# Kernel optimization log

Hardware: AMD Instinct MI355X
Metric: run time of the kernel (lower is better)

Reference implementation:

```python
import jax, jax.numpy as jnp
import numpy as np

NUM_HEADS = 4
CATEGORY_SIZE = 128
NUM_TOKENS = 64


def setup_inputs() -> dict:
    key = jax.random.key(0)
    k1, k2, k3 = jax.random.split(key, 3)
    b, n, c = 2, 65536, 192
    qkv = jax.random.normal(k1, (b, n, 3 * c), dtype=jnp.float32)
    sim = jax.random.normal(k2, (b, n, NUM_TOKENS), dtype=jnp.float32)
    proj_w = jax.random.normal(k3, (c, c), dtype=jnp.float32) * 0.02  # nn.Linear weight (out, in)
    proj_b = jnp.zeros((c,), dtype=jnp.float32)
    logit_scale = jnp.log(10.0) * jnp.ones((1, 1), dtype=jnp.float32)
    return {"qkv": qkv, "sim": sim, "proj_w": proj_w, "proj_b": proj_b,
            "logit_scale": logit_scale, "H": 256, "W": 256}


def reference(qkv, sim, proj_w, proj_b, logit_scale, H, W):
    b, n, c3 = qkv.shape
    c = c3 // 3
    hd = c // NUM_HEADS
    gs = min(n, CATEGORY_SIZE)
    ng = (n + gs - 1) // gs
    pad_n = ng * gs - n

    # cluster id per token, sort tokens by cluster (dynamic reorder)
    tk_id = jnp.argmax(sim, axis=-1)                    # (b, n) int
    sort_idx = jnp.argsort(tk_id, axis=-1)              # permutation
    rev_idx = jnp.argsort(sort_idx, axis=-1)            # inverse permutation (index_reverse)

    shuffled = jnp.take_along_axis(qkv, sort_idx[..., None], axis=1)  # (b, n, 3c)
    if pad_n > 0:
        pad = shuffled[:, n - pad_n:n][:, ::-1]         # torch.flip of tail
        shuffled = jnp.concatenate([shuffled, pad], axis=1)

    # (b, ng, gs, 3, nh, hd) -> (3, b, ng, nh, gs, hd)
    y = shuffled.reshape(b, ng, gs, 3, NUM_HEADS, hd)
    qkv_g = jnp.transpose(y, (3, 0, 1, 4, 2, 5))
    q, k, v = qkv_g[0], qkv_g[1], qkv_g[2]

    # clamped learned logit scale (no normalization in original code)
    scale = jnp.exp(jnp.minimum(logit_scale, jnp.log(1.0 / 0.01)))[0, 0]
    attn = jnp.einsum('bgnsd,bgntd->bgnst', q, k) * scale   # (b, ng, nh, gs, gs)
    attn = jax.nn.softmax(attn, axis=-1)
    out = jnp.einsum('bgnst,bgntd->bgnsd', attn, v)         # (b, ng, nh, gs, hd)

    out = jnp.transpose(out, (0, 1, 3, 2, 4)).reshape(b, ng * gs, c)[:, :n]
    x = jnp.take_along_axis(out, rev_idx[..., None], axis=1)  # unshuffle
    x = x @ proj_w.T + proj_b
    return x
```

## Files before the change

kernel.cpp:

```cpp
#include <hip/hip_runtime.h>

#define B_  2
#define N_  65536
#define C_  192
#define NH_ 4
#define HD_ 48
#define GS_ 128
#define NG_ 512
#define NTILES_ 256

typedef __attribute__((ext_vector_type(8))) short short8;
typedef __attribute__((ext_vector_type(4))) float f32x4;

__device__ __forceinline__ unsigned short f2bf(float f) {
    unsigned u = __float_as_uint(f);
    unsigned r = (u + 0x7FFFu + ((u >> 16) & 1u)) >> 16;
    return (unsigned short)r;
}
__device__ __forceinline__ float bf2f(unsigned short s) {
    return __uint_as_float(((unsigned)s) << 16);
}
__device__ __forceinline__ unsigned cvt_pk(float a, float b) {
    unsigned r;
    asm("v_cvt_pk_bf16_f32 %0, %1, %2" : "=v"(r) : "v"(a), "v"(b));
    return r;
}

__global__ __launch_bounds__(256) void argmax_kernel(const float* __restrict__ sim,
                                                     int* __restrict__ keys) {
    int lane  = threadIdx.x & 63;
    int token = blockIdx.x * 4 + (threadIdx.x >> 6);
    float v = sim[(size_t)token * 64 + lane];
    int idx = lane;
    #pragma unroll
    for (int m = 1; m < 64; m <<= 1) {
        float ov = __shfl_xor(v, m);
        int   oi = __shfl_xor(idx, m);
        if (ov > v || (ov == v && oi < idx)) { v = ov; idx = oi; }
    }
    if (lane == 0) keys[token] = idx;
}

__global__ __launch_bounds__(256) void hist_kernel(const int* __restrict__ keys,
                                                   int* __restrict__ counts) {
    __shared__ int hcnt[64];
    int tid  = threadIdx.x;
    int tile = blockIdx.x & (NTILES_ - 1);
    int bz   = blockIdx.x >> 8;
    if (tid < 64) hcnt[tid] = 0;
    __syncthreads();
    int k = keys[bz * N_ + tile * 256 + tid];
    atomicAdd(&hcnt[k], 1);
    __syncthreads();
    if (tid < 64) counts[(bz * NTILES_ + tile) * 64 + tid] = hcnt[tid];
}

__global__ __launch_bounds__(256) void scan_kernel(int* __restrict__ counts) {
    __shared__ int qsum[4][64];
    __shared__ int kbase[64];
    int bz = blockIdx.x;
    int k  = threadIdx.x & 63;
    int qt = threadIdx.x >> 6;
    int base_idx = (bz * NTILES_) * 64 + k;

    int sum = 0;
    #pragma unroll 8
    for (int t = qt * 64; t < qt * 64 + 64; ++t) sum += counts[base_idx + t * 64];
    qsum[qt][k] = sum;
    __syncthreads();

    if (qt == 0) {
        int tot = qsum[0][k] + qsum[1][k] + qsum[2][k] + qsum[3][k];
        int incl = tot;
        #pragma unroll
        for (int off = 1; off < 64; off <<= 1) {
            int v = __shfl_up(incl, off);
            if (k >= off) incl += v;
        }
        kbase[k] = incl - tot;
    }
    __syncthreads();

    int run = kbase[k];
    for (int q2 = 0; q2 < qt; ++q2) run += qsum[q2][k];
    #pragma unroll 8
    for (int t = qt * 64; t < qt * 64 + 64; ++t) {
        int idx = base_idx + t * 64;
        int c = counts[idx];
        counts[idx] = run;
        run += c;
    }
}

__global__ __launch_bounds__(256) void rank_kernel(const int* __restrict__ keys,
                                                   const int* __restrict__ counts,
                                                   int* __restrict__ sidx,
                                                   int* __restrict__ dest) {
    __shared__ int whist[4 * 64];
    int tid  = threadIdx.x;
    int tile = blockIdx.x & (NTILES_ - 1);
    int bz   = blockIdx.x >> 8;
    whist[tid] = 0;
    __syncthreads();

    int tok = tile * 256 + tid;
    int key = keys[bz * N_ + tok];
    int w = tid >> 6, lane = tid & 63;

    unsigned long long mask = ~0ull;
    #pragma unroll
    for (int b = 0; b < 6; ++b) {
        unsigned long long bb = __ballot((key >> b) & 1);
        mask &= ((key >> b) & 1) ? bb : ~bb;
    }
    unsigned long long lt = (lane == 0) ? 0ull : (~0ull >> (64 - lane));
    int rank = __popcll(mask & lt);
    if (rank == 0) whist[w * 64 + key] = __popcll(mask);
    __syncthreads();

    int base = counts[(bz * NTILES_ + tile) * 64 + key];
    for (int w2 = 0; w2 < w; ++w2) base += whist[w2 * 64 + key];
    int pos = base + rank;
    sidx[bz * N_ + pos] = tok;
    dest[bz * N_ + tok] = pos;
}

#define KP_STRIDE 104
#define P_STRIDE  136
#define VT_STRIDE 136
#define SM_VT   34816
#define SM_SIDX (SM_VT + 48*VT_STRIDE*2)
#define SM_SIZE (SM_SIDX + 512)

__global__ __launch_bounds__(256, 3) void attn_kernel(const float* __restrict__ qkv,
                                                      const float* __restrict__ lscale,
                                                      const int* __restrict__ sort_idx,
                                                      unsigned short* __restrict__ oattn) {
    __shared__ __align__(16) char smem[SM_SIZE];
    unsigned short* kp = (unsigned short*)smem;
    unsigned short* vt = (unsigned short*)(smem + SM_VT);
    int* sidx_s = (int*)(smem + SM_SIDX);

    int x  = blockIdx.x;
    int h  = x & 3;
    int g  = (x >> 2) & (NG_ - 1);
    int bz = x >> 11;
    int tid = threadIdx.x;

    if (tid < 128) sidx_s[tid] = sort_idx[bz * N_ + g * GS_ + tid];
    __syncthreads();

    int lane = tid & 63, wid = tid >> 6;
    int lr = lane & 15, lg = lane >> 4;
    int qt0 = wid * 2, qt1 = qt0 + 1;
    float scale = __expf(fminf(lscale[0], 4.60517019f));

    int r0s = lg * 8;
    int r1s = 16 + lg * 8;
    int r2s = (lg < 2) ? 32 + lg * 8 : (lg - 2) * 8;
    const float* q0p = qkv + (size_t)(bz * N_ + sidx_s[qt0 * 16 + lr]) * 576 + h * 48;
    const float* q1p = qkv + (size_t)(bz * N_ + sidx_s[qt1 * 16 + lr]) * 576 + h * 48;
    float4 qA0 = *(const float4*)(q0p + r0s), qA1 = *(const float4*)(q0p + r0s + 4);
    float4 qB0 = *(const float4*)(q0p + r1s), qB1 = *(const float4*)(q0p + r1s + 4);
    float4 qC0 = *(const float4*)(q0p + r2s), qC1 = *(const float4*)(q0p + r2s + 4);
    float4 pA0 = *(const float4*)(q1p + r0s), pA1 = *(const float4*)(q1p + r0s + 4);
    float4 pB0 = *(const float4*)(q1p + r1s), pB1 = *(const float4*)(q1p + r1s + 4);
    float4 pC0 = *(const float4*)(q1p + r2s), pC1 = *(const float4*)(q1p + r2s + 4);

    #pragma unroll
    for (int it = 0; it < 6; ++it) {
        int f = it * 256 + tid;
        int row = f / 12, piece = f - row * 12;
        float4 kf = *(const float4*)(qkv + (size_t)(bz * N_ + sidx_s[row]) * 576 + 192 + h * 48 + piece * 4);
        unsigned h01 = cvt_pk(kf.x, kf.y), h23 = cvt_pk(kf.z, kf.w);
        float hx = __uint_as_float(h01 << 16), hy = __uint_as_float(h01 & 0xFFFF0000u);
        float hz = __uint_as_float(h23 << 16), hw = __uint_as_float(h23 & 0xFFFF0000u);
        unsigned l01 = cvt_pk(kf.x - hx, kf.y - hy), l23 = cvt_pk(kf.z - hz, kf.w - hw);
        *(uint2*)(kp + row * KP_STRIDE + piece * 4)      = make_uint2(h01, h23);
        *(uint2*)(kp + row * KP_STRIDE + 48 + piece * 4) = make_uint2(l01, l23);
    }
    #pragma unroll
    for (int it = 0; it < 6; ++it) {
        int f = it * 256 + tid;
        int row = f / 12, piece = f - row * 12;
        float4 vf = *(const float4*)(qkv + (size_t)(bz * N_ + sidx_s[row]) * 576 + 384 + h * 48 + piece * 4);
        int d = piece * 4;
        vt[(d + 0) * VT_STRIDE + row] = f2bf(vf.x);
        vt[(d + 1) * VT_STRIDE + row] = f2bf(vf.y);
        vt[(d + 2) * VT_STRIDE + row] = f2bf(vf.z);
        vt[(d + 3) * VT_STRIDE + row] = f2bf(vf.w);
    }

    unsigned af0[5][4], af1[5][4];
    {
        float a0[8] = {qA0.x,qA0.y,qA0.z,qA0.w,qA1.x,qA1.y,qA1.z,qA1.w};
        float b0[8] = {qB0.x,qB0.y,qB0.z,qB0.w,qB1.x,qB1.y,qB1.z,qB1.w};
        float c0[8] = {qC0.x,qC0.y,qC0.z,qC0.w,qC1.x,qC1.y,qC1.z,qC1.w};
        float a1[8] = {pA0.x,pA0.y,pA0.z,pA0.w,pA1.x,pA1.y,pA1.z,pA1.w};
        float b1[8] = {pB0.x,pB0.y,pB0.z,pB0.w,pB1.x,pB1.y,pB1.z,pB1.w};
        float c1[8] = {pC0.x,pC0.y,pC0.z,pC0.w,pC1.x,pC1.y,pC1.z,pC1.w};
        #pragma unroll
        for (int j = 0; j < 8; ++j) {
            a0[j] *= scale; b0[j] *= scale; c0[j] *= scale;
            a1[j] *= scale; b1[j] *= scale; c1[j] *= scale;
        }
        #pragma unroll
        for (int w = 0; w < 4; ++w) {
            af0[0][w] = cvt_pk(a0[2*w], a0[2*w+1]);
            af1[0][w] = cvt_pk(a1[2*w], a1[2*w+1]);
            af0[3][w] = af0[0][w];
            af1[3][w] = af1[0][w];
            {
                unsigned t0 = cvt_pk(b0[2*w], b0[2*w+1]);
                float hx = __uint_as_float(t0 << 16), hy = __uint_as_float(t0 & 0xFFFF0000u);
                af0[2][w] = cvt_pk(b0[2*w] - hx, b0[2*w+1] - hy);
                unsigned t1 = cvt_pk(b1[2*w], b1[2*w+1]);
                float ix = __uint_as_float(t1 << 16), iy = __uint_as_float(t1 & 0xFFFF0000u);
                af1[2][w] = cvt_pk(b1[2*w] - ix, b1[2*w+1] - iy);
            }
            if (lg < 2) {
                af0[1][w] = cvt_pk(c0[2*w], c0[2*w+1]);
                af1[1][w] = cvt_pk(c1[2*w], c1[2*w+1]);
                af0[4][w] = af0[1][w];
                af1[4][w] = af1[1][w];
            } else {
                unsigned t0 = cvt_pk(c0[2*w], c0[2*w+1]);
                float hx = __uint_as_float(t0 << 16), hy = __uint_as_float(t0 & 0xFFFF0000u);
                af0[1][w] = cvt_pk(c0[2*w] - hx, c0[2*w+1] - hy);
                unsigned t1 = cvt_pk(c1[2*w], c1[2*w+1]);
                float ix = __uint_as_float(t1 << 16), iy = __uint_as_float(t1 & 0xFFFF0000u);
                af1[1][w] = cvt_pk(c1[2*w] - ix, c1[2*w+1] - iy);
                af0[4][w] = 0; af1[4][w] = 0;
            }
        }
    }
    __syncthreads();

    const int boffs[5] = { lg * 8, (32 + lg * 8) % 48, 16 + lg * 8,
                           48 + lg * 8, (lg < 2) ? 80 + lg * 8 : 48 };
    f32x4 acc0[8], acc1[8];
    #pragma unroll
    for (int kt = 0; kt < 8; ++kt) { acc0[kt] = (f32x4)0.f; acc1[kt] = (f32x4)0.f; }

    #pragma unroll
    for (int s = 0; s < 5; ++s) {
        union { short8 v; unsigned u[4]; } ua, ub;
        #pragma unroll
        for (int w = 0; w < 4; ++w) { ua.u[w] = af0[s][w]; ub.u[w] = af1[s][w]; }
        short8 a0 = ua.v, a1 = ub.v;
        #pragma unroll
        for (int kt = 0; kt < 8; ++kt) {
            short8 b = *(const short8*)(kp + (size_t)(kt * 16 + lr) * KP_STRIDE + boffs[s]);
            acc0[kt] = __builtin_amdgcn_mfma_f32_16x16x32_bf16(a0, b, acc0[kt], 0, 0, 0);
            acc1[kt] = __builtin_amdgcn_mfma_f32_16x16x32_bf16(a1, b, acc1[kt], 0, 0, 0);
        }
    }

    float inv0[4], inv1[4];
    {
        float mx0[4], mx1[4];
        #pragma unroll
        for (int r = 0; r < 4; ++r) { mx0[r] = -1e30f; mx1[r] = -1e30f; }
        #pragma unroll
        for (int kt = 0; kt < 8; ++kt)
            #pragma unroll
            for (int r = 0; r < 4; ++r) {
                mx0[r] = fmaxf(mx0[r], acc0[kt][r]);
                mx1[r] = fmaxf(mx1[r], acc1[kt][r]);
            }
        #pragma unroll
        for (int m = 1; m < 16; m <<= 1)
            #pragma unroll
            for (int r = 0; r < 4; ++r) {
                mx0[r] = fmaxf(mx0[r], __shfl_xor(mx0[r], m));
                mx1[r] = fmaxf(mx1[r], __shfl_xor(mx1[r], m));
            }
        float sm0[4] = {0.f,0.f,0.f,0.f}, sm1[4] = {0.f,0.f,0.f,0.f};
        #pragma unroll
        for (int kt = 0; kt < 8; ++kt)
            #pragma unroll
            for (int r = 0; r < 4; ++r) {
                float e0 = __expf(acc0[kt][r] - mx0[r]);
                float e1 = __expf(acc1[kt][r] - mx1[r]);
                acc0[kt][r] = e0; acc1[kt][r] = e1;
                sm0[r] += e0; sm1[r] += e1;
            }
        #pragma unroll
        for (int m = 1; m < 16; m <<= 1)
            #pragma unroll
            for (int r = 0; r < 4; ++r) {
                sm0[r] += __shfl_xor(sm0[r], m);
                sm1[r] += __shfl_xor(sm1[r], m);
            }
        #pragma unroll
        for (int r = 0; r < 4; ++r) { inv0[r] = 1.f / sm0[r]; inv1[r] = 1.f / sm1[r]; }
    }

    __syncthreads();

    #pragma unroll
    for (int kt = 0; kt < 8; ++kt)
        #pragma unroll
        for (int r = 0; r < 4; ++r) {
            kp[(size_t)(qt0 * 16 + lg * 4 + r) * P_STRIDE + kt * 16 + lr] = (unsigned short)cvt_pk(acc0[kt][r], acc0[kt][r]);
            kp[(size_t)(qt1 * 16 + lg * 4 + r) * P_STRIDE + kt * 16 + lr] = (unsigned short)cvt_pk(acc1[kt][r], acc1[kt][r]);
        }

    f32x4 o0[3], o1[3];
    #pragma unroll
    for (int dt = 0; dt < 3; ++dt) { o0[dt] = (f32x4)0.f; o1[dt] = (f32x4)0.f; }
    #pragma unroll
    for (int ks = 0; ks < 4; ++ks) {
        short8 a0 = *(const short8*)(kp + (size_t)(qt0 * 16 + lr) * P_STRIDE + ks * 32 + lg * 8);
        short8 a1 = *(const short8*)(kp + (size_t)(qt1 * 16 + lr) * P_STRIDE + ks * 32 + lg * 8);
        #pragma unroll
        for (int dt = 0; dt < 3; ++dt) {
            short8 bv = *(const short8*)(vt + (size_t)(dt * 16 + lr) * VT_STRIDE + ks * 32 + lg * 8);
            o0[dt] = __builtin_amdgcn_mfma_f32_16x16x32_bf16(a0, bv, o0[dt], 0, 0, 0);
            o1[dt] = __builtin_amdgcn_mfma_f32_16x16x32_bf16(a1, bv, o1[dt], 0, 0, 0);
        }
    }

    #pragma unroll
    for (int dt = 0; dt < 3; ++dt)
        #pragma unroll
        for (int r = 0; r < 4; ++r) {
            int row0 = qt0 * 16 + lg * 4 + r;
            int row1 = qt1 * 16 + lg * 4 + r;
            oattn[(size_t)(bz * N_ + g * GS_ + row0) * C_ + h * HD_ + dt * 16 + lr] =
                f2bf(o0[dt][r] * inv0[r]);
            oattn[(size_t)(bz * N_ + g * GS_ + row1) * C_ + h * HD_ + dt * 16 + lr] =
                f2bf(o1[dt][r] * inv1[r]);
        }
}

__global__ __launch_bounds__(256) void wconv_kernel(const float* __restrict__ W,
                                                    unsigned short* __restrict__ wbf) {
    int i = blockIdx.x * 256 + threadIdx.x;
    float4 f = ((const float4*)W)[i];
    uint2 p;
    p.x = (unsigned)f2bf(f.x) | ((unsigned)f2bf(f.y) << 16);
    p.y = (unsigned)f2bf(f.z) | ((unsigned)f2bf(f.w) << 16);
    ((uint2*)wbf)[i] = p;
}

__global__ __launch_bounds__(256) void proj2_kernel(const unsigned short* __restrict__ oattn,
                                                    const int* __restrict__ dest,
                                                    const unsigned short* __restrict__ wbf,
                                                    const float* __restrict__ bias,
                                                    float* __restrict__ out) {
    __shared__ int mpos[128];
    int tid = threadIdx.x;
    int m0  = blockIdx.x * 128;

    if (tid < 128) {
        int m = m0 + tid;
        int bz = m >> 16;
        mpos[tid] = bz * N_ + dest[m];
    }
    __syncthreads();

    int lane = tid & 63, wid = tid >> 6;
    int lr = lane & 15, lg = lane >> 4;
    int mt0 = wid * 2, mt1 = wid * 2 + 1;

    const unsigned short* xr0 = oattn + (size_t)mpos[mt0 * 16 + lr] * C_ + lg * 8;
    const unsigned short* xr1 = oattn + (size_t)mpos[mt1 * 16 + lr] * C_ + lg * 8;
    const unsigned short* wr  = wbf + (size_t)lr * C_ + lg * 8;

    f32x4 acc[2][12];
    #pragma unroll
    for (int mt = 0; mt < 2; ++mt)
        #pragma unroll
        for (int jt = 0; jt < 12; ++jt) acc[mt][jt] = (f32x4)0.f;

    #pragma unroll
    for (int ks = 0; ks < 6; ++ks) {
        short8 a0 = *(const short8*)(xr0 + ks * 32);
        short8 a1 = *(const short8*)(xr1 + ks * 32);
        #pragma unroll
        for (int jt = 0; jt < 12; ++jt) {
            short8 b = *(const short8*)(wr + (size_t)jt * 16 * C_ + ks * 32);
            acc[0][jt] = __builtin_amdgcn_mfma_f32_16x16x32_bf16(a0, b, acc[0][jt], 0, 0, 0);
            acc[1][jt] = __builtin_amdgcn_mfma_f32_16x16x32_bf16(a1, b, acc[1][jt], 0, 0, 0);
        }
    }

    #pragma unroll
    for (int jt = 0; jt < 12; ++jt) {
        int j = jt * 16 + lr;
        float bj = bias[j];
        #pragma unroll
        for (int r = 0; r < 4; ++r) {
            int row0 = m0 + mt0 * 16 + lg * 4 + r;
            int row1 = m0 + mt1 * 16 + lg * 4 + r;
            out[(size_t)row0 * C_ + j] = acc[0][jt][r] + bj;
            out[(size_t)row1 * C_ + j] = acc[1][jt][r] + bj;
        }
    }
}

extern "C" void kernel_launch(void* const* d_in, const int* in_sizes, int n_in,
                              void* d_out, int out_size, void* d_ws, size_t ws_size,
                              hipStream_t stream) {
    const float* qkv    = (const float*)d_in[0];
    const float* sim    = (const float*)d_in[1];
    const float* proj_w = (const float*)d_in[2];
    const float* proj_b = (const float*)d_in[3];
    const float* lscale = (const float*)d_in[4];
    float* out = (float*)d_out;

    char* ws = (char*)d_ws;
    int* keys   = (int*)(ws);
    int* dest   = (int*)(ws + 524288);
    int* sidx   = (int*)(ws + 1048576);
    int* counts = (int*)(ws + 1572864);
    unsigned short* oattn = (unsigned short*)(ws + 1703936);
    unsigned short* wbf   = (unsigned short*)(ws + 1703936 + 50331648);

    argmax_kernel<<<32768, 256, 0, stream>>>(sim, keys);
    hist_kernel<<<B_ * NTILES_, 256, 0, stream>>>(keys, counts);
    scan_kernel<<<B_, 256, 0, stream>>>(counts);
    rank_kernel<<<B_ * NTILES_, 256, 0, stream>>>(keys, counts, sidx, dest);
    wconv_kernel<<<36, 256, 0, stream>>>(proj_w, wbf);
    attn_kernel<<<B_ * NG_ * NH_, 256, 0, stream>>>(qkv, lscale, sidx, oattn);
    proj2_kernel<<<(B_ * N_) / 128, 256, 0, stream>>>(oattn, dest, wbf, proj_b, out);
}
```

Before: 216.4 us.

## Keep softmax probabilities in registers, swap QK operands, reorder block mapping, scatter proj output

The QK^T MFMA now takes K as the A operand and Q as B, so each lane holds a full probability column. That column is normalized, packed to bf16 in registers, and fed straight into 16x16x16 MFMAs for PV. This removes the LDS round-trip for P, a __syncthreads, and the 16-lane shuffle reductions. The smaller LDS footprint allows launch bounds of 4 blocks per SM, and block indices are remapped so that 8 consecutive blocks share the same head. proj2 now reads oattn contiguously in sorted order and scatters its output rows through sidx, which removes the dest array and its writes in rank_kernel. The risks are more register pressure and scattered fp32 output writes.

Result: no change. 218.7 us (+1.0%).

```diff
diff --git a/kernel.cpp b/kernel.cpp
--- a/kernel.cpp
+++ b/kernel.cpp
@@ -10,6 +10,7 @@
 #define NTILES_ 256
 
 typedef __attribute__((ext_vector_type(8))) short short8;
+typedef __attribute__((ext_vector_type(4))) short short4v;
 typedef __attribute__((ext_vector_type(4))) float f32x4;
 
 __device__ __forceinline__ unsigned short f2bf(float f) {
@@ -24,6 +25,22 @@
     unsigned r;
     asm("v_cvt_pk_bf16_f32 %0, %1, %2" : "=v"(r) : "v"(a), "v"(b));
     return r;
+}
+
+#if defined(__has_builtin)
+#if __has_builtin(__builtin_amdgcn_mfma_f32_16x16x16bf16_1k)
+#define HAVE_MFMA16_1K 1
+#endif
+#endif
+__device__ __forceinline__ f32x4 mfma16(short4v a, short4v b, f32x4 c) {
+#ifdef HAVE_MFMA16_1K
+    return __builtin_amdgcn_mfma_f32_16x16x16bf16_1k(a, b, c, 0, 0, 0);
+#else
+    f32x4 d;
+    asm volatile("v_mfma_f32_16x16x16_bf16 %0, %1, %2, %3"
+                 : "=&v"(d) : "v"(a), "v"(b), "v"(c));
+    return d;
+#endif
 }
 
 __global__ __launch_bounds__(256) void argmax_kernel(const float* __restrict__ sim,
@@ -94,8 +111,7 @@
 
 __global__ __launch_bounds__(256) void rank_kernel(const int* __restrict__ keys,
                                                    const int* __restrict__ counts,
-                                                   int* __restrict__ sidx,
-                                                   int* __restrict__ dest) {
+                                                   int* __restrict__ sidx) {
     __shared__ int whist[4 * 64];
     int tid  = threadIdx.x;
     int tile = blockIdx.x & (NTILES_ - 1);
@@ -122,29 +138,28 @@
     for (int w2 = 0; w2 < w; ++w2) base += whist[w2 * 64 + key];
     int pos = base + rank;
     sidx[bz * N_ + pos] = tok;
-    dest[bz * N_ + tok] = pos;
 }
 
 #define KP_STRIDE 104
-#define P_STRIDE  136
-#define VT_STRIDE 136
-#define SM_VT   34816
-#define SM_SIDX (SM_VT + 48*VT_STRIDE*2)
-#define SM_SIZE (SM_SIDX + 512)
-
-__global__ __launch_bounds__(256, 3) void attn_kernel(const float* __restrict__ qkv,
+#define VT_STRIDE 132
+#define KP_BYTES  (128 * KP_STRIDE * 2)
+#define VT_BYTES  (48 * VT_STRIDE * 2)
+#define SM_SIZE   (KP_BYTES + VT_BYTES + 512)
+
+__global__ __launch_bounds__(256, 4) void attn_kernel(const float* __restrict__ qkv,
                                                       const float* __restrict__ lscale,
                                                       const int* __restrict__ sort_idx,
                                                       unsigned short* __restrict__ oattn) {
     __shared__ __align__(16) char smem[SM_SIZE];
     unsigned short* kp = (unsigned short*)smem;
-    unsigned short* vt = (unsigned short*)(smem + SM_VT);
-    int* sidx_s = (int*)(smem + SM_SIDX);
+    unsigned short* vt = (unsigned short*)(smem + KP_BYTES);
+    int* sidx_s = (int*)(smem + KP_BYTES + VT_BYTES);
 
     int x  = blockIdx.x;
-    int h  = x & 3;
-    int g  = (x >> 2) & (NG_ - 1);
-    int bz = x >> 11;
+    int gg = (x & 7) | ((x >> 5) << 3);
+    int h  = (x >> 3) & 3;
+    int g  = gg & (NG_ - 1);
+    int bz = gg >> 9;
     int tid = threadIdx.x;
 
     if (tid < 128) sidx_s[tid] = sort_idx[bz * N_ + g * GS_ + tid];
@@ -247,77 +262,61 @@
         union { short8 v; unsigned u[4]; } ua, ub;
         #pragma unroll
         for (int w = 0; w < 4; ++w) { ua.u[w] = af0[s][w]; ub.u[w] = af1[s][w]; }
-        short8 a0 = ua.v, a1 = ub.v;
+        short8 b0 = ua.v, b1 = ub.v;
         #pragma unroll
         for (int kt = 0; kt < 8; ++kt) {
-            short8 b = *(const short8*)(kp + (size_t)(kt * 16 + lr) * KP_STRIDE + boffs[s]);
-            acc0[kt] = __builtin_amdgcn_mfma_f32_16x16x32_bf16(a0, b, acc0[kt], 0, 0, 0);
-            acc1[kt] = __builtin_amdgcn_mfma_f32_16x16x32_bf16(a1, b, acc1[kt], 0, 0, 0);
-        }
-    }
-
-    float inv0[4], inv1[4];
+            short8 a = *(const short8*)(kp + (size_t)(kt * 16 + lr) * KP_STRIDE + boffs[s]);
+            acc0[kt] = __builtin_amdgcn_mfma_f32_16x16x32_bf16(a, b0, acc0[kt], 0, 0, 0);
+            acc1[kt] = __builtin_amdgcn_mfma_f32_16x16x32_bf16(a, b1, acc1[kt], 0, 0, 0);
+        }
+    }
+
+    short4v pf0[8], pf1[8];
     {
-        float mx0[4], mx1[4];
-        #pragma unroll
-        for (int r = 0; r < 4; ++r) { mx0[r] = -1e30f; mx1[r] = -1e30f; }
+        float m0v = -1e30f, m1v = -1e30f;
         #pragma unroll
         for (int kt = 0; kt < 8; ++kt)
             #pragma unroll
             for (int r = 0; r < 4; ++r) {
-                mx0[r] = fmaxf(mx0[r], acc0[kt][r]);
-                mx1[r] = fmaxf(mx1[r], acc1[kt][r]);
+                m0v = fmaxf(m0v, acc0[kt][r]);
+                m1v = fmaxf(m1v, acc1[kt][r]);
             }
-        #pragma unroll
-        for (int m = 1; m < 16; m <<= 1)
-            #pragma unroll
-            for (int r = 0; r < 4; ++r) {
-                mx0[r] = fmaxf(mx0[r], __shfl_xor(mx0[r], m));
-                mx1[r] = fmaxf(mx1[r], __shfl_xor(mx1[r], m));
-            }
-        float sm0[4] = {0.f,0.f,0.f,0.f}, sm1[4] = {0.f,0.f,0.f,0.f};
+        m0v = fmaxf(m0v, __shfl_xor(m0v, 16)); m0v = fmaxf(m0v, __shfl_xor(m0v, 32));
+        m1v = fmaxf(m1v, __shfl_xor(m1v, 16)); m1v = fmaxf(m1v, __shfl_xor(m1v, 32));
+        float s0v = 0.f, s1v = 0.f;
         #pragma unroll
         for (int kt = 0; kt < 8; ++kt)
             #pragma unroll
             for (int r = 0; r < 4; ++r) {
-                float e0 = __expf(acc0[kt][r] - mx0[r]);
-                float e1 = __expf(acc1[kt][r] - mx1[r]);
+                float e0 = __expf(acc0[kt][r] - m0v);
+                float e1 = __expf(acc1[kt][r] - m1v);
                 acc0[kt][r] = e0; acc1[kt][r] = e1;
-                sm0[r] += e0; sm1[r] += e1;
+                s0v += e0; s1v += e1;
             }
-        #pragma unroll
-        for (int m = 1; m < 16; m <<= 1)
-            #pragma unroll
-            for (int r = 0; r < 4; ++r) {
-                sm0[r] += __shfl_xor(sm0[r], m);
-                sm1[r] += __shfl_xor(sm1[r], m);
-            }
-        #pragma unroll
-        for (int r = 0; r < 4; ++r) { inv0[r] = 1.f / sm0[r]; inv1[r] = 1.f / sm1[r]; }
-    }
-
-    __syncthreads();
-
-    #pragma unroll
-    for (int kt = 0; kt < 8; ++kt)
-        #pragma unroll
-        for (int r = 0; r < 4; ++r) {
-            kp[(size_t)(qt0 * 16 + lg * 4 + r) * P_STRIDE + kt * 16 + lr] = (unsigned short)cvt_pk(acc0[kt][r], acc0[kt][r]);
-            kp[(size_t)(qt1 * 16 + lg * 4 + r) * P_STRIDE + kt * 16 + lr] = (unsigned short)cvt_pk(acc1[kt][r], acc1[kt][r]);
-        }
+        s0v += __shfl_xor(s0v, 16); s0v += __shfl_xor(s0v, 32);
+        s1v += __shfl_xor(s1v, 16); s1v += __shfl_xor(s1v, 32);
+        float inv0 = 1.f / s0v, inv1 = 1.f / s1v;
+        #pragma unroll
+        for (int kt = 0; kt < 8; ++kt) {
+            union { short4v v; unsigned u[2]; } u0, u1;
+            u0.u[0] = cvt_pk(acc0[kt][0] * inv0, acc0[kt][1] * inv0);
+            u0.u[1] = cvt_pk(acc0[kt][2] * inv0, acc0[kt][3] * inv0);
+            u1.u[0] = cvt_pk(acc1[kt][0] * inv1, acc1[kt][1] * inv1);
+            u1.u[1] = cvt_pk(acc1[kt][2] * inv1, acc1[kt][3] * inv1);
+            pf0[kt] = u0.v; pf1[kt] = u1.v;
+        }
+    }
 
     f32x4 o0[3], o1[3];
     #pragma unroll
     for (int dt = 0; dt < 3; ++dt) { o0[dt] = (f32x4)0.f; o1[dt] = (f32x4)0.f; }
     #pragma unroll
-    for (int ks = 0; ks < 4; ++ks) {
-        short8 a0 = *(const short8*)(kp + (size_t)(qt0 * 16 + lr) * P_STRIDE + ks * 32 + lg * 8);
-        short8 a1 = *(const short8*)(kp + (size_t)(qt1 * 16 + lr) * P_STRIDE + ks * 32 + lg * 8);
+    for (int kt = 0; kt < 8; ++kt) {
         #pragma unroll
         for (int dt = 0; dt < 3; ++dt) {
-            short8 bv = *(const short8*)(vt + (size_t)(dt * 16 + lr) * VT_STRIDE + ks * 32 + lg * 8);
-            o0[dt] = __builtin_amdgcn_mfma_f32_16x16x32_bf16(a0, bv, o0[dt], 0, 0, 0);
-            o1[dt] = __builtin_amdgcn_mfma_f32_16x16x32_bf16(a1, bv, o1[dt], 0, 0, 0);
+            short4v vf = *(const short4v*)(vt + (size_t)(dt * 16 + lr) * VT_STRIDE + kt * 16 + lg * 4);
+            o0[dt] = mfma16(pf0[kt], vf, o0[dt]);
+            o1[dt] = mfma16(pf1[kt], vf, o1[dt]);
         }
     }
 
@@ -327,10 +326,8 @@
         for (int r = 0; r < 4; ++r) {
             int row0 = qt0 * 16 + lg * 4 + r;
             int row1 = qt1 * 16 + lg * 4 + r;
-            oattn[(size_t)(bz * N_ + g * GS_ + row0) * C_ + h * HD_ + dt * 16 + lr] =
-                f2bf(o0[dt][r] * inv0[r]);
-            oattn[(size_t)(bz * N_ + g * GS_ + row1) * C_ + h * HD_ + dt * 16 + lr] =
-                f2bf(o1[dt][r] * inv1[r]);
+            oattn[(size_t)(bz * N_ + g * GS_ + row0) * C_ + h * HD_ + dt * 16 + lr] = f2bf(o0[dt][r]);
+            oattn[(size_t)(bz * N_ + g * GS_ + row1) * C_ + h * HD_ + dt * 16 + lr] = f2bf(o1[dt][r]);
         }
 }
 
@@ -345,18 +342,18 @@
 }
 
 __global__ __launch_bounds__(256) void proj2_kernel(const unsigned short* __restrict__ oattn,
-                                                    const int* __restrict__ dest,
+                                                    const int* __restrict__ sidx,
                                                     const unsigned short* __restrict__ wbf,
                                                     const float* __restrict__ bias,
                                                     float* __restrict__ out) {
-    __shared__ int mpos[128];
+    __shared__ int mout[128];
     int tid = threadIdx.x;
-    int m0  = blockIdx.x * 128;
+    int s0  = blockIdx.x * 128;
 
     if (tid < 128) {
-        int m = m0 + tid;
-        int bz = m >> 16;
-        mpos[tid] = bz * N_ + dest[m];
+        int s = s0 + tid;
+        int bz = s >> 16;
+        mout[tid] = bz * N_ + sidx[s];
     }
     __syncthreads();
 
@@ -364,8 +361,8 @@
     int lr = lane & 15, lg = lane >> 4;
     int mt0 = wid * 2, mt1 = wid * 2 + 1;
 
-    const unsigned short* xr0 = oattn + (size_t)mpos[mt0 * 16 + lr] * C_ + lg * 8;
-    const unsigned short* xr1 = oattn + (size_t)mpos[mt1 * 16 + lr] * C_ + lg * 8;
+    const unsigned short* xr0 = oattn + (size_t)(s0 + mt0 * 16 + lr) * C_ + lg * 8;
+    const unsigned short* xr1 = oattn + (size_t)(s0 + mt1 * 16 + lr) * C_ + lg * 8;
     const unsigned short* wr  = wbf + (size_t)lr * C_ + lg * 8;
 
     f32x4 acc[2][12];
@@ -392,8 +389,8 @@
         float bj = bias[j];
         #pragma unroll
         for (int r = 0; r < 4; ++r) {
-            int row0 = m0 + mt0 * 16 + lg * 4 + r;
-            int row1 = m0 + mt1 * 16 + lg * 4 + r;
+            int row0 = mout[mt0 * 16 + lg * 4 + r];
+            int row1 = mout[mt1 * 16 + lg * 4 + r];
             out[(size_t)row0 * C_ + j] = acc[0][jt][r] + bj;
             out[(size_t)row1 * C_ + j] = acc[1][jt][r] + bj;
         }
@@ -412,7 +409,6 @@
 
     char* ws = (char*)d_ws;
     int* keys   = (int*)(ws);
-    int* dest   = (int*)(ws + 524288);
     int* sidx   = (int*)(ws + 1048576);
     int* counts = (int*)(ws + 1572864);
     unsigned short* oattn = (unsigned short*)(ws + 1703936);
@@ -421,8 +417,8 @@
     argmax_kernel<<<32768, 256, 0, stream>>>(sim, keys);
     hist_kernel<<<B_ * NTILES_, 256, 0, stream>>>(keys, counts);
     scan_kernel<<<B_, 256, 0, stream>>>(counts);
-    rank_kernel<<<B_ * NTILES_, 256, 0, stream>>>(keys, counts, sidx, dest);
+    rank_kernel<<<B_ * NTILES_, 256, 0, stream>>>(keys, counts, sidx);
     wconv_kernel<<<36, 256, 0, stream>>>(proj_w, wbf);
     attn_kernel<<<B_ * NG_ * NH_, 256, 0, stream>>>(qkv, lscale, sidx, oattn);
-    proj2_kernel<<<(B_ * N_) / 128, 256, 0, stream>>>(oattn, dest, wbf, proj_b, out);
-}
+    proj2_kernel<<<(B_ * N_) / 128, 256, 0, stream>>>(oattn, sidx, wbf, proj_b, out);
+}
```
